# Kernel optimization log

Hardware: AMD Instinct MI355X
Metric: run time of the kernel (lower is better)

The kernel has to match this reference:

```python
import jax, jax.numpy as jnp
import numpy as np


def smooth_l1(x, y):
    d = jnp.abs(x - y)
    return jnp.where(d < 1.0, 0.5 * d * d, d - 0.5)


def setup_inputs() -> dict:
    key = jax.random.key(0)
    k1, k2, k3 = jax.random.split(key, 3)
    B, T, N, D = 4, 28, 1024, 3
    X_v = jax.random.normal(k1, (B, T, N, D), dtype=jnp.float32)
    target_X_v = jax.random.normal(k2, (B, T, N, D), dtype=jnp.float32)
    weights = jax.random.uniform(k3, (B, T), dtype=jnp.float32)
    return {"X_v": X_v, "target_X_v": target_X_v, "weights": weights}


def reference(X_v, target_X_v, weights):
    B = X_v.shape[0]
    # Pairwise squared distances [B,T,N,N] via ||p||^2 + ||t||^2 - 2 p.t
    pn = jnp.sum(X_v * X_v, axis=-1)                 # [B,T,N]
    tn = jnp.sum(target_X_v * target_X_v, axis=-1)   # [B,T,N]
    dist = (pn[..., :, None] + tn[..., None, :]
            - 2.0 * jnp.einsum('btnd,btmd->btnm', X_v, target_X_v))
    minv = jnp.argmin(dist, axis=-1)                 # [B,T,N] int
    # gather nearest target point for each pred point
    tagp = jnp.take_along_axis(target_X_v, minv[..., None], axis=2)  # [B,T,N,3]
    # per-(b,t) mean smooth-L1 over N points x 3 coords
    loss_bt = jnp.mean(smooth_l1(X_v, tagp), axis=(-2, -1))          # [B,T]
    loss = jnp.sum(loss_bt * weights) / B

    prec = jnp.mean(X_v, axis=2)        # [B,T,3]
    tarc = jnp.mean(target_X_v, axis=2) # [B,T,3]
    lossc = jnp.sum(smooth_l1(prec, tarc)) / (B * 3)
    return (loss, lossc)
```

## Files before the change

kernel.cpp:

```cpp
#include <hip/hip_runtime.h>

constexpr int Bc = 4;
constexpr int Tc = 28;
constexpr int Nc = 1024;
constexpr int Dc = 3;
constexpr int BT = Bc * Tc;
constexpr int TQ = 256;
constexpr int NQ = Nc / TQ;


__device__ __forceinline__ float sl1(float d) {
    d = fabsf(d);
    return d < 1.0f ? 0.5f * d * d : d - 0.5f;
}

__device__ __forceinline__ float pack_key(float v, unsigned m) {
    return __uint_as_float((__float_as_uint(v) & 0xFFFFFC00u) | m);
}

__global__ __launch_bounds__(256) void chamfer_kernel(
    const float* __restrict__ X, const float* __restrict__ Tg,
    float4* __restrict__ bestkP, float* __restrict__ out)
{
    __shared__ float4 sT4[TQ];

    const int bt  = blockIdx.x >> 2;
    const int th  = blockIdx.x & 3;
    const int tid = threadIdx.x;

    if (blockIdx.x == 0 && tid < 2) out[tid] = 0.0f;

    const float4* x4 = (const float4*)(X + (size_t)bt * (Nc * Dc));
    const float4 a0 = x4[3 * tid + 0];
    const float4 a1 = x4[3 * tid + 1];
    const float4 a2 = x4[3 * tid + 2];
    const float cx[4] = {-2.f * a0.x, -2.f * a0.w, -2.f * a1.z, -2.f * a2.y};
    const float cy[4] = {-2.f * a0.y, -2.f * a1.x, -2.f * a1.w, -2.f * a2.z};
    const float cz[4] = {-2.f * a0.z, -2.f * a1.y, -2.f * a2.x, -2.f * a2.w};

    if (tid < 64) {
        const float4* tg4 = (const float4*)(Tg + (size_t)bt * (Nc * Dc) + th * (TQ * 3));
        const float4 r0 = tg4[3 * tid + 0];
        const float4 r1 = tg4[3 * tid + 1];
        const float4 r2 = tg4[3 * tid + 2];
        sT4[4 * tid + 0] = make_float4(r0.x, r0.y, r0.z, fmaf(r0.x, r0.x, fmaf(r0.y, r0.y, r0.z * r0.z)));
        sT4[4 * tid + 1] = make_float4(r0.w, r1.x, r1.y, fmaf(r0.w, r0.w, fmaf(r1.x, r1.x, r1.y * r1.y)));
        sT4[4 * tid + 2] = make_float4(r1.z, r1.w, r2.x, fmaf(r1.z, r1.z, fmaf(r1.w, r1.w, r2.x * r2.x)));
        sT4[4 * tid + 3] = make_float4(r2.y, r2.z, r2.w, fmaf(r2.y, r2.y, fmaf(r2.z, r2.z, r2.w * r2.w)));
    }
    __syncthreads();

    const unsigned mgBase = (unsigned)(th * TQ);
    float best[4] = {3.4e38f, 3.4e38f, 3.4e38f, 3.4e38f};

    constexpr int PF = 4;
    float4 bufA[PF], bufB[PF];
    #pragma unroll
    for (int j = 0; j < PF; ++j) bufA[j] = sT4[j];

    for (int m0 = 0; m0 < TQ; m0 += 2 * PF) {
        #pragma unroll
        for (int j = 0; j < PF; ++j) bufB[j] = sT4[m0 + PF + j];
        #pragma unroll
        for (int j = 0; j < PF; j += 2) {
            const float4 t0 = bufA[j], t1 = bufA[j + 1];
            const unsigned mg0 = mgBase + m0 + j, mg1 = mg0 + 1;
            #pragma unroll
            for (int k = 0; k < 4; ++k) {
                float v0 = fmaf(cx[k], t0.x, fmaf(cy[k], t0.y, fmaf(cz[k], t0.z, t0.w)));
                float v1 = fmaf(cx[k], t1.x, fmaf(cy[k], t1.y, fmaf(cz[k], t1.z, t1.w)));
                best[k] = fminf(fminf(pack_key(v0, mg0), pack_key(v1, mg1)), best[k]);
            }
        }
        #pragma unroll
        for (int j = 0; j < PF; ++j) bufA[j] = sT4[(m0 + 2 * PF + j) & (TQ - 1)];
        #pragma unroll
        for (int j = 0; j < PF; j += 2) {
            const float4 t0 = bufB[j], t1 = bufB[j + 1];
            const unsigned mg0 = mgBase + m0 + PF + j, mg1 = mg0 + 1;
            #pragma unroll
            for (int k = 0; k < 4; ++k) {
                float v0 = fmaf(cx[k], t0.x, fmaf(cy[k], t0.y, fmaf(cz[k], t0.z, t0.w)));
                float v1 = fmaf(cx[k], t1.x, fmaf(cy[k], t1.y, fmaf(cz[k], t1.z, t1.w)));
                best[k] = fminf(fminf(pack_key(v0, mg0), pack_key(v1, mg1)), best[k]);
            }
        }
    }

    bestkP[((size_t)th * BT + bt) * 256 + tid] = make_float4(best[0], best[1], best[2], best[3]);
}

__global__ __launch_bounds__(256) void gather_finalize_kernel(
    const float* __restrict__ X, const float* __restrict__ Tg,
    const float* __restrict__ W,
    const float4* __restrict__ bestkP, float* __restrict__ out)
{
    __shared__ float sred[4][8];
    const int bt  = blockIdx.x;
    const int tid = threadIdx.x;
    const size_t rb = (size_t)bt * 256 + tid;

    float4 bk = bestkP[rb];
    #pragma unroll
    for (int q = 1; q < NQ; ++q) {
        const float4 k2 = bestkP[(size_t)q * BT * 256 + rb];
        bk.x = fminf(bk.x, k2.x);
        bk.y = fminf(bk.y, k2.y);
        bk.z = fminf(bk.z, k2.z);
        bk.w = fminf(bk.w, k2.w);
    }
    const int idx[4] = {
        (int)(__float_as_uint(bk.x) & 1023u),
        (int)(__float_as_uint(bk.y) & 1023u),
        (int)(__float_as_uint(bk.z) & 1023u),
        (int)(__float_as_uint(bk.w) & 1023u)
    };

    const float4* x4 = (const float4*)(X + (size_t)bt * (Nc * Dc));
    const float4 a0 = x4[3 * tid + 0];
    const float4 a1 = x4[3 * tid + 1];
    const float4 a2 = x4[3 * tid + 2];
    const float px[4] = {a0.x, a0.w, a1.z, a2.y};
    const float py[4] = {a0.y, a1.x, a1.w, a2.z};
    const float pz[4] = {a0.z, a1.y, a2.x, a2.w};

    const float4* t4 = (const float4*)(Tg + (size_t)bt * (Nc * Dc));
    const float4 r0 = t4[3 * tid + 0];
    const float4 r1 = t4[3 * tid + 1];
    const float4 r2 = t4[3 * tid + 2];

    const float* tb = Tg + (size_t)bt * (Nc * Dc);
    float s = 0.0f;
    #pragma unroll
    for (int k = 0; k < 4; ++k) {
        const float tx = tb[idx[k] * 3 + 0];
        const float ty = tb[idx[k] * 3 + 1];
        const float tz = tb[idx[k] * 3 + 2];
        s += sl1(px[k] - tx) + sl1(py[k] - ty) + sl1(pz[k] - tz);
    }

    float vals[7] = {
        s,
        px[0] + px[1] + px[2] + px[3],
        py[0] + py[1] + py[2] + py[3],
        pz[0] + pz[1] + pz[2] + pz[3],
        r0.x + r0.w + r1.z + r2.y,
        r0.y + r1.x + r1.w + r2.z,
        r0.z + r1.y + r2.x + r2.w
    };
    const int lane = tid & 63, wid = tid >> 6;
    #pragma unroll
    for (int k = 0; k < 7; ++k) {
        float v = vals[k];
        #pragma unroll
        for (int off = 32; off; off >>= 1) v += __shfl_down(v, off, 64);
        if (lane == 0) sred[wid][k] = v;
    }
    __syncthreads();
    if (tid == 0) {
        float tot[7];
        #pragma unroll
        for (int k = 0; k < 7; ++k)
            tot[k] = sred[0][k] + sred[1][k] + sred[2][k] + sred[3][k];
        atomicAdd(out, tot[0] * W[bt] * (1.0f / (Nc * Dc)) * (1.0f / Bc));
        const float inv = 1.0f / Nc;
        float lc = sl1((tot[1] - tot[4]) * inv)
                 + sl1((tot[2] - tot[5]) * inv)
                 + sl1((tot[3] - tot[6]) * inv);
        atomicAdd(out + 1, lc * (1.0f / (Bc * Dc)));
    }
}

extern "C" void kernel_launch(void* const* d_in, const int* in_sizes, int n_in,
                              void* d_out, int out_size, void* d_ws, size_t ws_size,
                              hipStream_t stream) {
    const float* X  = (const float*)d_in[0];
    const float* Tg = (const float*)d_in[1];
    const float* W  = (const float*)d_in[2];
    float* out = (float*)d_out;

    float4* bestkP = (float4*)d_ws;

    chamfer_kernel<<<BT * NQ, 256, 0, stream>>>(X, Tg, bestkP, out);
    gather_finalize_kernel<<<BT, 256, 0, stream>>>(X, Tg, W, bestkP, out);
}
```

Baseline: 80.17 us.

## Fuse chamfer search and gather-finalize via atomicMin and last-block counter

Merges the two kernels into one. Each quarter-block folds its per-point best keys into a global array with atomicMin, using an order-preserving float-to-unsigned mapping. A per-(b,t) arrival counter picks the last block, which then does the gather, the smooth-L1 reduction and the centroid loss. This removes the second kernel launch and the partial-key round trip, but adds two memsets per call, global atomics and threadfences.

```diff
diff --git a/kernel.cpp b/kernel.cpp
--- a/kernel.cpp
+++ b/kernel.cpp
@@ -18,17 +18,28 @@
     return __uint_as_float((__float_as_uint(v) & 0xFFFFFC00u) | m);
 }
 
-__global__ __launch_bounds__(256) void chamfer_kernel(
+__device__ __forceinline__ unsigned fkey_to_u(float f) {
+    unsigned b = __float_as_uint(f);
+    return (b & 0x80000000u) ? ~b : (b | 0x80000000u);
+}
+__device__ __forceinline__ int u_to_idx(unsigned u) {
+    unsigned b = (u & 0x80000000u) ? (u & 0x7FFFFFFFu) : ~u;
+    return (int)(b & 1023u);
+}
+
+__global__ __launch_bounds__(256) void chamfer_fused_kernel(
     const float* __restrict__ X, const float* __restrict__ Tg,
-    float4* __restrict__ bestkP, float* __restrict__ out)
+    const float* __restrict__ W,
+    unsigned* __restrict__ amin, unsigned* __restrict__ cnt,
+    float* __restrict__ out)
 {
     __shared__ float4 sT4[TQ];
+    __shared__ float sred[4][8];
+    __shared__ unsigned s_old;
 
     const int bt  = blockIdx.x >> 2;
     const int th  = blockIdx.x & 3;
     const int tid = threadIdx.x;
-
-    if (blockIdx.x == 0 && tid < 2) out[tid] = 0.0f;
 
     const float4* x4 = (const float4*)(X + (size_t)bt * (Nc * Dc));
     const float4 a0 = x4[3 * tid + 0];
@@ -87,47 +98,29 @@
         }
     }
 
-    bestkP[((size_t)th * BT + bt) * 256 + tid] = make_float4(best[0], best[1], best[2], best[3]);
-}
+    unsigned* ab = amin + (size_t)bt * Nc + 4 * tid;
+    atomicMin(ab + 0, fkey_to_u(best[0]));
+    atomicMin(ab + 1, fkey_to_u(best[1]));
+    atomicMin(ab + 2, fkey_to_u(best[2]));
+    atomicMin(ab + 3, fkey_to_u(best[3]));
 
-__global__ __launch_bounds__(256) void gather_finalize_kernel(
-    const float* __restrict__ X, const float* __restrict__ Tg,
-    const float* __restrict__ W,
-    const float4* __restrict__ bestkP, float* __restrict__ out)
-{
-    __shared__ float sred[4][8];
-    const int bt  = blockIdx.x;
-    const int tid = threadIdx.x;
-    const size_t rb = (size_t)bt * 256 + tid;
+    __threadfence();
+    __syncthreads();
+    if (tid == 0) s_old = atomicAdd(&cnt[bt], 1u);
+    __syncthreads();
+    if (s_old != (unsigned)(NQ - 2)) return;
 
-    float4 bk = bestkP[rb];
-    #pragma unroll
-    for (int q = 1; q < NQ; ++q) {
-        const float4 k2 = bestkP[(size_t)q * BT * 256 + rb];
-        bk.x = fminf(bk.x, k2.x);
-        bk.y = fminf(bk.y, k2.y);
-        bk.z = fminf(bk.z, k2.z);
-        bk.w = fminf(bk.w, k2.w);
-    }
-    const int idx[4] = {
-        (int)(__float_as_uint(bk.x) & 1023u),
-        (int)(__float_as_uint(bk.y) & 1023u),
-        (int)(__float_as_uint(bk.z) & 1023u),
-        (int)(__float_as_uint(bk.w) & 1023u)
-    };
+    __threadfence();
 
-    const float4* x4 = (const float4*)(X + (size_t)bt * (Nc * Dc));
-    const float4 a0 = x4[3 * tid + 0];
-    const float4 a1 = x4[3 * tid + 1];
-    const float4 a2 = x4[3 * tid + 2];
+    const unsigned k0 = atomicAdd(ab + 0, 0u);
+    const unsigned k1 = atomicAdd(ab + 1, 0u);
+    const unsigned k2 = atomicAdd(ab + 2, 0u);
+    const unsigned k3 = atomicAdd(ab + 3, 0u);
+    const int idx[4] = {u_to_idx(k0), u_to_idx(k1), u_to_idx(k2), u_to_idx(k3)};
+
     const float px[4] = {a0.x, a0.w, a1.z, a2.y};
     const float py[4] = {a0.y, a1.x, a1.w, a2.z};
     const float pz[4] = {a0.z, a1.y, a2.x, a2.w};
-
-    const float4* t4 = (const float4*)(Tg + (size_t)bt * (Nc * Dc));
-    const float4 r0 = t4[3 * tid + 0];
-    const float4 r1 = t4[3 * tid + 1];
-    const float4 r2 = t4[3 * tid + 2];
 
     const float* tb = Tg + (size_t)bt * (Nc * Dc);
     float s = 0.0f;
@@ -138,6 +131,11 @@
         const float tz = tb[idx[k] * 3 + 2];
         s += sl1(px[k] - tx) + sl1(py[k] - ty) + sl1(pz[k] - tz);
     }
+
+    const float4* t4 = (const float4*)tb;
+    const float4 r0 = t4[3 * tid + 0];
+    const float4 r1 = t4[3 * tid + 1];
+    const float4 r2 = t4[3 * tid + 2];
 
     float vals[7] = {
         s,
@@ -179,8 +177,11 @@
     const float* W  = (const float*)d_in[2];
     float* out = (float*)d_out;
 
-    float4* bestkP = (float4*)d_ws;
+    unsigned* amin = (unsigned*)d_ws;
+    unsigned* cnt  = amin + (size_t)BT * Nc;
 
-    chamfer_kernel<<<BT * NQ, 256, 0, stream>>>(X, Tg, bestkP, out);
-    gather_finalize_kernel<<<BT, 256, 0, stream>>>(X, Tg, W, bestkP, out);
+    hipMemsetAsync(amin, 0xFF, ((size_t)BT * Nc + BT) * sizeof(unsigned), stream);
+    hipMemsetAsync(out, 0, 2 * sizeof(float), stream);
+
+    chamfer_fused_kernel<<<BT * NQ, 256, 0, stream>>>(X, Tg, W, amin, cnt, out);
 }
```

Result: slower. 122.0 us (+52.2%).
